# Kernel tuning notes

Measured on AMD Instinct MI355X. Metric: run time of the kernel, lower is better.

The kernel has to match this reference:

```python
import jax, jax.numpy as jnp
import numpy as np

OUT_SIZE = 7
SAMPLE_NUM = 2
FINEST_SCALE = 56.0
STRIDES = (4, 8, 16, 32)
IMG_H, IMG_W = 800.0, 1216.0


def roi_align(feat, rois, out_size, spatial_scale, sr):
    """Vectorized RoIAlign (aligned=False / mmdet legacy semantics).
    feat: [B,C,H,W]; rois: [K,5] (batch_idx, x1, y1, x2, y2). Returns [K,C,out,out]."""
    B, C, H, W = feat.shape
    K = rois.shape[0]
    ft = jnp.transpose(feat, (0, 2, 3, 1))  # [B,H,W,C] for channel-last gathers
    b = rois[:, 0].astype(jnp.int32)
    x1 = rois[:, 1] * spatial_scale
    y1 = rois[:, 2] * spatial_scale
    x2 = rois[:, 3] * spatial_scale
    y2 = rois[:, 4] * spatial_scale
    roi_w = jnp.maximum(x2 - x1, 1.0)
    roi_h = jnp.maximum(y2 - y1, 1.0)
    bin_w = roi_w / out_size
    bin_h = roi_h / out_size
    G = out_size * sr  # sample grid points per spatial dim
    g = (jnp.arange(G, dtype=feat.dtype) + 0.5) / sr  # sub-bin centers in bin units
    ys = y1[:, None] + g[None, :] * bin_h[:, None]  # [K,G]
    xs = x1[:, None] + g[None, :] * bin_w[:, None]  # [K,G]
    # validity (points outside [-1, H]/[-1, W] contribute 0)
    vy = (ys >= -1.0) & (ys <= H)
    vx = (xs >= -1.0) & (xs <= W)
    valid = vy[:, :, None] & vx[:, None, :]  # [K,G,G]
    # clamp into the map, then bilinear interpolate
    ysc = jnp.clip(ys, 0.0, H - 1)
    xsc = jnp.clip(xs, 0.0, W - 1)
    y0 = jnp.floor(ysc)
    x0 = jnp.floor(xsc)
    ly = ysc - y0
    lx = xsc - x0
    y0i = y0.astype(jnp.int32)
    x0i = x0.astype(jnp.int32)

    def gather(yi, xi):  # yi:[K,G], xi:[K,G] -> [K,G,G,C]
        yc = jnp.clip(yi, 0, H - 1)
        xc = jnp.clip(xi, 0, W - 1)
        return ft[b[:, None, None], yc[:, :, None], xc[:, None, :], :]

    wy0 = (1.0 - ly)[:, :, None, None]
    wy1 = ly[:, :, None, None]
    wx0 = (1.0 - lx)[:, None, :, None]
    wx1 = lx[:, None, :, None]
    val = (gather(y0i, x0i) * (wy0 * wx0)
           + gather(y0i, x0i + 1) * (wy0 * wx1)
           + gather(y0i + 1, x0i) * (wy1 * wx0)
           + gather(y0i + 1, x0i + 1) * (wy1 * wx1))  # [K,G,G,C]
    val = val * valid[..., None]
    # average the sr x sr samples in each output bin
    val = val.reshape(K, out_size, sr, out_size, sr, C).mean(axis=(2, 4))
    return jnp.transpose(val, (0, 3, 1, 2))  # [K,C,out,out]


def map_roi_levels(rois, num_levels):
    scale = jnp.sqrt((rois[:, 3] - rois[:, 1] + 1.0) * (rois[:, 4] - rois[:, 2] + 1.0))
    lvl = jnp.floor(jnp.log2(scale / FINEST_SCALE + 1e-6))
    return jnp.clip(lvl, 0, num_levels - 1).astype(jnp.int32)


def setup_inputs() -> dict:
    key = jax.random.key(0)
    ks = jax.random.split(key, 10)
    feat0 = jax.random.normal(ks[0], (2, 256, 200, 304), dtype=jnp.float32)
    feat1 = jax.random.normal(ks[1], (2, 256, 100, 152), dtype=jnp.float32)
    feat2 = jax.random.normal(ks[2], (2, 256, 50, 76), dtype=jnp.float32)
    feat3 = jax.random.normal(ks[3], (2, 256, 25, 38), dtype=jnp.float32)
    K = 1024
    b = jax.random.randint(ks[4], (K,), 0, 2).astype(jnp.float32)
    # log-uniform box sizes in [16, 600] px so all 4 FPN levels are used
    logw = jax.random.uniform(ks[5], (K,), minval=np.log(16.0), maxval=np.log(600.0))
    logh = jax.random.uniform(ks[6], (K,), minval=np.log(16.0), maxval=np.log(600.0))
    w = jnp.exp(logw)
    h = jnp.exp(logh)
    cx = jax.random.uniform(ks[7], (K,), minval=0.0, maxval=IMG_W)
    cy = jax.random.uniform(ks[8], (K,), minval=0.0, maxval=IMG_H)
    x1 = jnp.clip(cx - w / 2, 0.0, IMG_W - 2.0)
    y1 = jnp.clip(cy - h / 2, 0.0, IMG_H - 2.0)
    x2 = jnp.clip(cx + w / 2, x1 + 1.0, IMG_W - 1.0)
    y2 = jnp.clip(cy + h / 2, y1 + 1.0, IMG_H - 1.0)
    rois = jnp.stack([b, x1, y1, x2, y2], axis=1).astype(jnp.float32)
    return {"feat0": feat0, "feat1": feat1, "feat2": feat2, "feat3": feat3, "rois": rois}


def reference(feat0, feat1, feat2, feat3, rois):
    feats = [feat0, feat1, feat2, feat3]
    num_levels = len(feats)
    lvls = map_roi_levels(rois, num_levels)  # [K]
    K = rois.shape[0]
    C = feats[0].shape[1]
    out = jnp.zeros((K, C, OUT_SIZE, OUT_SIZE), dtype=feats[0].dtype)
    for i in range(num_levels):
        pooled = roi_align(feats[i], rois, OUT_SIZE, 1.0 / STRIDES[i], SAMPLE_NUM)
        out = out + jnp.where((lvls == i)[:, None, None, None], pooled, 0.0)
    return out
```

## Files before the change

### kernel.cpp

```cpp
#include <hip/hip_runtime.h>
#include <math.h>


#define OUT_SZ 7
#define NCH 256
#define NBINS 49
#define CGC 64
#define NGROUPS 4
#define LDS_N 1920

template<int VSH>
__device__ __forceinline__ void roi_group(
    const float* __restrict__ cbase, int CLrel, int HW, int H, int W,
    float x1, float y1, float bw, float bh,
    int t, float* __restrict__ outk, float (*lds)[LDS_N])
{
    const int V = 1 << VSH;
    const float fH = (float)H, fW = (float)W;

    float xf0 = fminf(fmaxf(x1 + 0.25f * bw, 0.0f), fW - 1.0f);
    float xfl = fminf(fmaxf(x1 + 6.75f * bw, 0.0f), fW - 1.0f);
    int xa = (int)floorf(xf0);
    int xb = min((int)floorf(xfl) + 1, W - 1);
    float yf0 = fminf(fmaxf(y1 + 0.25f * bh, 0.0f), fH - 1.0f);
    float yfl = fminf(fmaxf(y1 + 6.75f * bh, 0.0f), fH - 1.0f);
    int ya = (int)floorf(yf0);
    int yb = min((int)floorf(yfl) + 1, H - 1);

    int axa    = xa & ~(V - 1);
    int cpr    = ((xb - axa) >> VSH) + 1;
    int rowlen = cpr << VSH;
    int stride = rowlen + (((rowlen & 31) == 0) ? V : 0);
    int Rows   = yb - ya + 1;
    int C      = Rows * cpr;

    {
        int sent = Rows * stride;
        if (t == 0) { lds[0][sent] = 0.0f; lds[1][sent] = 0.0f; }
        int padw = stride - rowlen;
        if (padw) {
            int np = Rows * padw;
            for (int z = t; z < np; z += 256) {
                int zr = z / padw, zc = z - zr * padw;
                int idx = zr * stride + rowlen + zc;
                lds[0][idx] = 0.0f;
                lds[1][idx] = 0.0f;
            }
        }
    }

    int q0 = (t + 60) & 255;
    int goff[2], loff[2];
    bool act[2];
#pragma unroll
    for (int i = 0; i < 2; ++i) {
        int q = q0 + 256 * i;
        act[i] = q < C;
        int qq = act[i] ? q : 0;
        int r  = qq / cpr;
        int j  = qq - r * cpr;
        int rowbase = (ya + r) * W;
        int rel  = rowbase + axa + (j << VSH);
        int relc = min(rel, CLrel);
        goff[i] = relc;
        loff[i] = r * stride + (relc - rowbase - axa);
    }

    int bin = t >> 2;
    int s   = t & 3;
    int oy  = bin / OUT_SZ;
    int ox  = bin - oy * OUT_SZ;

    float xs  = x1 + ((float)(2 * ox + (s & 1)) + 0.5f) * 0.5f * bw;
    float ysv = y1 + ((float)(2 * oy + (s >> 1)) + 0.5f) * 0.5f * bh;
    bool vall = (xs >= -1.0f) && (xs <= fW) && (ysv >= -1.0f) && (ysv <= fH);

    float xc = fminf(fmaxf(xs, 0.0f), fW - 1.0f);
    float yc = fminf(fmaxf(ysv, 0.0f), fH - 1.0f);
    float xflr = floorf(xc), yflr = floorf(yc);
    int x0 = (int)xflr, y0 = (int)yflr;
    float lx = xc - xflr, ly = yc - yflr;

    int p0 = (y0 - ya) * stride + (x0 - axa);
    int ry = min(y0 + 1 - ya, Rows - 1);
    int p1 = ry * stride + (x0 - axa);

    float w00 = (1.0f - ly) * (1.0f - lx);
    float w01 = (1.0f - ly) * lx;
    float w10 = ly * (1.0f - lx);
    float w11 = ly * lx;

    auto ldchunk = [&](const float* p, int i) -> float4 {
        if (!act[i]) return make_float4(0.f, 0.f, 0.f, 0.f);
        if (VSH == 2) return *(const float4*)(p + goff[i]);
        float2 h2 = *(const float2*)(p + goff[i]);
        return make_float4(h2.x, h2.y, 0.f, 0.f);
    };
    auto stchunk = [&](float* dst, int i, float4 v) {
        if (act[i]) {
            if (VSH == 2) *(float4*)(dst + loff[i]) = v;
            else          *(float2*)(dst + loff[i]) = make_float2(v.x, v.y);
        }
    };

    float4 pv0[2], pv1[2], pv2[2], pv3[2], t0[2];
    t0[0]  = ldchunk(cbase, 0);
    pv1[0] = ldchunk(cbase + (size_t)HW, 0);
    pv2[0] = ldchunk(cbase + 2 * (size_t)HW, 0);
    pv3[0] = ldchunk(cbase + 3 * (size_t)HW, 0);
    pv0[0] = ldchunk(cbase + 4 * (size_t)HW, 0);
    if (C > 256) {
        t0[1]  = ldchunk(cbase, 1);
        pv1[1] = ldchunk(cbase + (size_t)HW, 1);
        pv2[1] = ldchunk(cbase + 2 * (size_t)HW, 1);
        pv3[1] = ldchunk(cbase + 3 * (size_t)HW, 1);
        pv0[1] = ldchunk(cbase + 4 * (size_t)HW, 1);
    }
    stchunk(lds[0], 0, t0[0]);
    if (C > 256) stchunk(lds[0], 1, t0[1]);
    __syncthreads();

#define ITER(k, PV)                                                     \
    {                                                                   \
        const int c = cc + (k);                                         \
        if (c + 1 < CGC) {                                              \
            float* dst = lds[((k) + 1) & 1];                            \
            stchunk(dst, 0, PV[0]);                                     \
            if (C > 256) stchunk(dst, 1, PV[1]);                        \
        }                                                               \
        if (c + 5 < CGC) {                                              \
            const float* pn = cbase + (size_t)(c + 5) * HW;             \
            PV[0] = ldchunk(pn, 0);                                     \
            if (C > 256) PV[1] = ldchunk(pn, 1);                        \
        }                                                               \
        if (t < 196) {                                                  \
            const float* L = lds[(k) & 1];                              \
            float v00 = L[p0];                                          \
            float v01 = L[p0 + 1];                                      \
            float v10 = L[p1];                                          \
            float v11 = L[p1 + 1];                                      \
            float val = vall ? (v00 * w00 + v01 * w01 + v10 * w10 +     \
                                v11 * w11)                              \
                             : 0.0f;                                    \
            val += __shfl_xor(val, 1, 64);                              \
            val += __shfl_xor(val, 2, 64);                              \
            if (s == 0) outk[c * NBINS + bin] = val * 0.25f;            \
        }                                                               \
        __syncthreads();                                                \
    }

    for (int cc = 0; cc < CGC; cc += 4) {
        ITER(0, pv1)
        ITER(1, pv2)
        ITER(2, pv3)
        ITER(3, pv0)
    }
#undef ITER
}

__global__ __launch_bounds__(256, 8)
void roi_align_fused(const float* __restrict__ f0, const float* __restrict__ f1,
                     const float* __restrict__ f2, const float* __restrict__ f3,
                     const float* __restrict__ rois,
                     float* __restrict__ out)
{
    __shared__ __align__(16) float lds[2][LDS_N];

    const int k = blockIdx.x;
    const int g = blockIdx.y;
    const int t = threadIdx.x;

    float rb   = rois[k * 5 + 0];
    float rix1 = rois[k * 5 + 1];
    float riy1 = rois[k * 5 + 2];
    float rix2 = rois[k * 5 + 3];
    float riy2 = rois[k * 5 + 4];

    float scale = sqrtf((rix2 - rix1 + 1.0f) * (riy2 - riy1 + 1.0f));
    int lvl = (int)floorf(log2f(scale * (1.0f / 56.0f) + 1e-6f));
    lvl = lvl < 0 ? 0 : (lvl > 3 ? 3 : lvl);

    float ss = 1.0f / (float)(4 << lvl);
    float x1 = rix1 * ss, y1 = riy1 * ss;
    float rw = fmaxf(rix2 * ss - x1, 1.0f);
    float rh = fmaxf(riy2 * ss - y1, 1.0f);
    float bw = rw * (1.0f / OUT_SZ);
    float bh = rh * (1.0f / OUT_SZ);
    const int H = 800  >> (2 + lvl);
    const int W = 1216 >> (2 + lvl);

    const float* fb = (lvl == 0) ? f0 : (lvl == 1) ? f1 : (lvl == 2) ? f2 : f3;
    const int HW  = H * W;
    const int TOT = 2 * NCH * HW;
    const int base_off = ((int)rb * NCH + g * CGC) * HW;
    const float* cbase = fb + base_off;
    float* outk = out + ((size_t)k * NCH + (size_t)(g * CGC)) * NBINS;

    if (W & 3) {
        int CLrel = TOT - base_off - (CGC - 1) * HW - 2;
        roi_group<1>(cbase, CLrel, HW, H, W, x1, y1, bw, bh, t, outk, lds);
    } else {
        int CLrel = TOT - base_off - (CGC - 1) * HW - 4;
        roi_group<2>(cbase, CLrel, HW, H, W, x1, y1, bw, bh, t, outk, lds);
    }
}

extern "C" void kernel_launch(void* const* d_in, const int* in_sizes, int n_in,
                              void* d_out, int out_size, void* d_ws, size_t ws_size,
                              hipStream_t stream)
{
    const float* f0   = (const float*)d_in[0];
    const float* f1   = (const float*)d_in[1];
    const float* f2   = (const float*)d_in[2];
    const float* f3   = (const float*)d_in[3];
    const float* rois = (const float*)d_in[4];
    float* out = (float*)d_out;

    int K = in_sizes[4] / 5;
    if (K <= 0) return;

    roi_align_fused<<<dim3(K, NGROUPS), 256, 0, stream>>>(f0, f1, f2, f3, rois, out);
}
```

Baseline: 305.6 us.

## Alternate blocks between direct global gather and LDS-staged RoIAlign paths

Adds a second RoIAlign path that gathers the bilinear sample points straight from global memory. Each wavefront handles one channel at a time and each lane handles one bin, with no LDS and no barriers. Blocks alternate between this path and the existing LDS-staged path according to the parity of (k+g). The mix is meant to balance memory-latency-bound and barrier-bound work across the GPU. It adds a heterogeneous workload within one grid, and the direct path does uncoalesced scattered loads.

```diff
diff --git a/kernel.cpp b/kernel.cpp
--- a/kernel.cpp
+++ b/kernel.cpp
@@ -120,11 +120,11 @@
     if (C > 256) stchunk(lds[0], 1, t0[1]);
     __syncthreads();
 
-#define ITER(k, PV)                                                     \
+#define ITER(kk, PV)                                                    \
     {                                                                   \
-        const int c = cc + (k);                                         \
+        const int c = cc + (kk);                                        \
         if (c + 1 < CGC) {                                              \
-            float* dst = lds[((k) + 1) & 1];                            \
+            float* dst = lds[((kk) + 1) & 1];                           \
             stchunk(dst, 0, PV[0]);                                     \
             if (C > 256) stchunk(dst, 1, PV[1]);                        \
         }                                                               \
@@ -134,7 +134,7 @@
             if (C > 256) PV[1] = ldchunk(pn, 1);                        \
         }                                                               \
         if (t < 196) {                                                  \
-            const float* L = lds[(k) & 1];                              \
+            const float* L = lds[(kk) & 1];                             \
             float v00 = L[p0];                                          \
             float v01 = L[p0 + 1];                                      \
             float v10 = L[p1];                                          \
@@ -158,11 +158,87 @@
 #undef ITER
 }
 
+__device__ __forceinline__ void roi_gather_direct(
+    const float* __restrict__ cbase, float* __restrict__ outk,
+    int HW, int H, int W,
+    float x1, float y1, float bw, float bh, int t)
+{
+    const int w    = t >> 6;
+    const int lane = t & 63;
+    const float fH = (float)H, fW = (float)W;
+
+    if (lane >= NBINS) return;
+    const int bin = lane;
+    const int oy = bin / OUT_SZ;
+    const int ox = bin - oy * OUT_SZ;
+
+    float lx[2], fvx[2]; int cx[2];
+#pragma unroll
+    for (int j = 0; j < 2; ++j) {
+        float xs = x1 + ((float)(2 * ox + j) + 0.5f) * 0.5f * bw;
+        fvx[j] = (xs >= -1.0f && xs <= fW) ? 1.0f : 0.0f;
+        float xc = fminf(fmaxf(xs, 0.0f), fW - 1.0f);
+        int x0 = (int)floorf(xc);
+        x0 = min(x0, W - 2);
+        lx[j] = xc - (float)x0;
+        cx[j] = x0;
+    }
+    float ly[2], fvy[2]; int ry[2];
+#pragma unroll
+    for (int i = 0; i < 2; ++i) {
+        float ysv = y1 + ((float)(2 * oy + i) + 0.5f) * 0.5f * bh;
+        fvy[i] = (ysv >= -1.0f && ysv <= fH) ? 1.0f : 0.0f;
+        float yc = fminf(fmaxf(ysv, 0.0f), fH - 1.0f);
+        int y0 = (int)floorf(yc);
+        y0 = min(y0, H - 2);
+        ly[i] = yc - (float)y0;
+        ry[i] = y0;
+    }
+    float wv00 = fvy[0] * fvx[0], wv01 = fvy[0] * fvx[1];
+    float wv10 = fvy[1] * fvx[0], wv11 = fvy[1] * fvx[1];
+
+    int off[8];
+#pragma unroll
+    for (int r = 0; r < 4; ++r) {
+        int row = ry[r >> 1] + (r & 1);
+        off[2 * r + 0] = row * W + cx[0];
+        off[2 * r + 1] = row * W + cx[1];
+    }
+
+    const float* chp = cbase + (size_t)w * HW;
+    float* outp = outk + (size_t)w * NBINS + bin;
+
+#pragma unroll 2
+    for (int i = 0; i < 16; ++i) {
+        float v0[8], v1[8];
+#pragma unroll
+        for (int q = 0; q < 8; ++q) {
+            v0[q] = chp[off[q]];
+            v1[q] = chp[off[q] + 1];
+        }
+        float h[8];
+#pragma unroll
+        for (int q = 0; q < 8; ++q)
+            h[q] = fmaf(lx[q & 1], v1[q] - v0[q], v0[q]);
+
+        float s00 = fmaf(ly[0], h[2] - h[0], h[0]);
+        float s01 = fmaf(ly[0], h[3] - h[1], h[1]);
+        float s10 = fmaf(ly[1], h[6] - h[4], h[4]);
+        float s11 = fmaf(ly[1], h[7] - h[5], h[5]);
+
+        float acc = wv00 * s00 + wv01 * s01 + wv10 * s10 + wv11 * s11;
+        *outp = acc * 0.25f;
+
+        chp  += 4 * (size_t)HW;
+        outp += 4 * NBINS;
+    }
+}
+
 __global__ __launch_bounds__(256, 8)
-void roi_align_fused(const float* __restrict__ f0, const float* __restrict__ f1,
-                     const float* __restrict__ f2, const float* __restrict__ f3,
-                     const float* __restrict__ rois,
-                     float* __restrict__ out)
+void roi_align_hybrid(const float* __restrict__ f0, const float* __restrict__ f1,
+                      const float* __restrict__ f2, const float* __restrict__ f3,
+                      const float* __restrict__ rois,
+                      float* __restrict__ out)
 {
     __shared__ __align__(16) float lds[2][LDS_N];
 
@@ -196,12 +272,16 @@
     const float* cbase = fb + base_off;
     float* outk = out + ((size_t)k * NCH + (size_t)(g * CGC)) * NBINS;
 
-    if (W & 3) {
-        int CLrel = TOT - base_off - (CGC - 1) * HW - 2;
-        roi_group<1>(cbase, CLrel, HW, H, W, x1, y1, bw, bh, t, outk, lds);
+    if (((k + g) & 1) == 0) {
+        roi_gather_direct(cbase, outk, HW, H, W, x1, y1, bw, bh, t);
     } else {
-        int CLrel = TOT - base_off - (CGC - 1) * HW - 4;
-        roi_group<2>(cbase, CLrel, HW, H, W, x1, y1, bw, bh, t, outk, lds);
+        if (W & 3) {
+            int CLrel = TOT - base_off - (CGC - 1) * HW - 2;
+            roi_group<1>(cbase, CLrel, HW, H, W, x1, y1, bw, bh, t, outk, lds);
+        } else {
+            int CLrel = TOT - base_off - (CGC - 1) * HW - 4;
+            roi_group<2>(cbase, CLrel, HW, H, W, x1, y1, bw, bh, t, outk, lds);
+        }
     }
 }
 
@@ -219,5 +299,5 @@
     int K = in_sizes[4] / 5;
     if (K <= 0) return;
 
-    roi_align_fused<<<dim3(K, NGROUPS), 256, 0, stream>>>(f0, f1, f2, f3, rois, out);
+    roi_align_hybrid<<<dim3(K, NGROUPS), 256, 0, stream>>>(f0, f1, f2, f3, rois, out);
 }
```

After: 327.4 us. 1.07x slower.
